# Optimization experiments

Measured on AMD Instinct MI355X. Metric: run time of the kernel, lower is better.

Reference implementation:

```python
import jax, jax.numpy as jnp
import numpy as np

D_MODEL = 1024
NUM_HEADS = 16
HEAD_DIM = D_MODEL // NUM_HEADS
FFN_HIDDEN = 4096
EPS = 1e-5


def setup_inputs() -> dict:
    key = jax.random.key(0)
    ks = jax.random.split(key, 7)
    s = 0.02
    return {
        "x": jax.random.normal(ks[0], (2, 2048, D_MODEL), dtype=jnp.float32),
        "W_qkv": jax.random.normal(ks[1], (D_MODEL, 3 * D_MODEL), dtype=jnp.float32) * s,
        "b_qkv": jnp.zeros((3 * D_MODEL,), dtype=jnp.float32),
        "W_o": jax.random.normal(ks[2], (D_MODEL, D_MODEL), dtype=jnp.float32) * s,
        "b_o": jnp.zeros((D_MODEL,), dtype=jnp.float32),
        "gamma1": jnp.ones((D_MODEL,), dtype=jnp.float32),
        "beta1": jnp.zeros((D_MODEL,), dtype=jnp.float32),
        "W1": jax.random.normal(ks[3], (D_MODEL, FFN_HIDDEN), dtype=jnp.float32) * s,
        "b1": jnp.zeros((FFN_HIDDEN,), dtype=jnp.float32),
        "W2": jax.random.normal(ks[4], (FFN_HIDDEN, D_MODEL), dtype=jnp.float32) * s,
        "b2": jnp.zeros((D_MODEL,), dtype=jnp.float32),
        "gamma2": jnp.ones((D_MODEL,), dtype=jnp.float32),
        "beta2": jnp.zeros((D_MODEL,), dtype=jnp.float32),
    }


def _layernorm(x, gamma, beta):
    mean = jnp.mean(x, axis=-1, keepdims=True)
    var = jnp.mean((x - mean) ** 2, axis=-1, keepdims=True)
    return gamma * (x - mean) / jnp.sqrt(var + EPS) + beta


def reference(x, W_qkv, b_qkv, W_o, b_o, gamma1, beta1, W1, b1, W2, b2, gamma2, beta2):
    B, S, D = x.shape
    # ---- multi-head attention ----
    qkv = x @ W_qkv + b_qkv                       # [B,S,3D]
    qkv = qkv.reshape(B, S, NUM_HEADS, 3 * HEAD_DIM).transpose(0, 2, 1, 3)  # [B,H,S,3hd]
    q, k, v = jnp.split(qkv, 3, axis=-1)          # each [B,H,S,hd]
    scores = jnp.einsum("bhqd,bhkd->bhqk", q, k) / np.sqrt(HEAD_DIM)
    attn = jax.nn.softmax(scores, axis=-1)
    vals = jnp.einsum("bhqk,bhkd->bhqd", attn, v)
    vals = vals.transpose(0, 2, 1, 3).reshape(B, S, D)
    attn_out = vals @ W_o + b_o
    # dropout disabled (eval mode)
    h = _layernorm(attn_out + x, gamma1, beta1)
    # ---- position-wise FFN (dropout before relu per source, disabled) ----
    ffn = jax.nn.relu(h @ W1 + b1) @ W2 + b2
    return _layernorm(ffn + h, gamma2, beta2)
```

## Files before the change

### kernel.cpp

```cpp
#include <hip/hip_runtime.h>
#include <stdint.h>

typedef float v4f __attribute__((ext_vector_type(4)));
typedef __bf16 v8bf __attribute__((ext_vector_type(8)));
typedef __bf16 v4bf __attribute__((ext_vector_type(4)));
typedef unsigned short v8us __attribute__((ext_vector_type(8)));
typedef unsigned short v4us __attribute__((ext_vector_type(4)));

__device__ __forceinline__ float b2f(unsigned short u) {
    union { float f; uint32_t i; } x; x.i = ((uint32_t)u) << 16; return x.f;
}
__device__ __forceinline__ unsigned short f2b(float f) {
    union { float f; uint32_t u; } x; x.f = f;
    uint32_t r = x.u + 0x7fffu + ((x.u >> 16) & 1u);
    return (unsigned short)(r >> 16);
}

__device__ __forceinline__ void gload16(const unsigned short* g, unsigned short* l) {
    __builtin_amdgcn_global_load_lds(
        (const __attribute__((address_space(1))) void*)g,
        (__attribute__((address_space(3))) void*)l,
        16, 0, 0);
}

__global__ __launch_bounds__(256) void convert_f32_bf16(
    const float* __restrict__ src, unsigned short* __restrict__ dst)
{
    int i = (blockIdx.x * 256 + threadIdx.x) * 4;
    float4 v = *(const float4*)&src[i];
    v4us o = {f2b(v.x), f2b(v.y), f2b(v.z), f2b(v.w)};
    *(v4us*)&dst[i] = o;
}

__global__ __launch_bounds__(256) void transpose_to_bt(
    const float* __restrict__ W, unsigned short* __restrict__ WT, int K, int N)
{
    __shared__ unsigned short t[64][65];
    const int kb = blockIdx.y * 64, nb = blockIdx.x * 64;
    const int r = threadIdx.x >> 4, c4 = (threadIdx.x & 15) * 4;
    #pragma unroll
    for (int i = 0; i < 4; ++i) {
        int k = r + i * 16;
        float4 v = *(const float4*)&W[(size_t)(kb + k) * N + nb + c4];
        t[c4 + 0][k] = f2b(v.x);
        t[c4 + 1][k] = f2b(v.y);
        t[c4 + 2][k] = f2b(v.z);
        t[c4 + 3][k] = f2b(v.w);
    }
    __syncthreads();
    #pragma unroll
    for (int i = 0; i < 4; ++i) {
        int n = r + i * 16;
        v4us o = {t[n][c4], t[n][c4 + 1], t[n][c4 + 2], t[n][c4 + 3]};
        *(v4us*)&WT[(size_t)(nb + n) * K + kb + c4] = o;
    }
}

__device__ __forceinline__ void xcd_swizzle(int& bm, int& bn) {
    int NB = gridDim.x, MB = gridDim.y;
    int flat = blockIdx.x + NB * blockIdx.y;
    int xcd = flat & 7, j = flat >> 3;
    int MBand = MB >> 3;
    bm = xcd * MBand + (j % MBand);
    bn = j / MBand;
}

template<int SPLIT_V>
__global__ __launch_bounds__(256) void gemm_bt(
    const unsigned short* __restrict__ A, const unsigned short* __restrict__ BT,
    const float* __restrict__ bias, unsigned short* __restrict__ C,
    unsigned short* __restrict__ VT, int M, int N, int K, int relu)
{
    __shared__ __align__(16) unsigned short sA[2][128 * 32];
    __shared__ __align__(16) unsigned short sB[2][128 * 32];
    const int tid  = threadIdx.x;
    const int wave = tid >> 6, lane = tid & 63;
    const int wm = wave >> 1, wn = wave & 1;
    const int quad = lane >> 4, l16 = lane & 15;
    int bm, bn;
    xcd_swizzle(bm, bn);

    const int srow = lane >> 2, scol = (lane & 3) * 8;
    const unsigned short* ga0 = A  + (size_t)(bm * 128 + (wave * 2 + 0) * 16 + srow) * K + scol;
    const unsigned short* ga1 = A  + (size_t)(bm * 128 + (wave * 2 + 1) * 16 + srow) * K + scol;
    const unsigned short* gb0 = BT + (size_t)(bn * 128 + (wave * 2 + 0) * 16 + srow) * K + scol;
    const unsigned short* gb1 = BT + (size_t)(bn * 128 + (wave * 2 + 1) * 16 + srow) * K + scol;
    const int o0 = (wave * 2 + 0) * 512 + lane * 8;
    const int o1 = (wave * 2 + 1) * 512 + lane * 8;

    v8us aR[2][2], bR[2][2];
    #pragma unroll
    for (int c = 0; c < 2; ++c) {
        aR[c][0] = *(const v8us*)(ga0 + c * 32);
        aR[c][1] = *(const v8us*)(ga1 + c * 32);
        bR[c][0] = *(const v8us*)(gb0 + c * 32);
        bR[c][1] = *(const v8us*)(gb1 + c * 32);
    }

    v4f acc[4][4];
    #pragma unroll
    for (int i = 0; i < 4; ++i)
        #pragma unroll
        for (int j = 0; j < 4; ++j)
            acc[i][j] = (v4f){0.f, 0.f, 0.f, 0.f};

    for (int kt = 0; kt < K; kt += 64) {
        __syncthreads();
        #pragma unroll
        for (int c = 0; c < 2; ++c) {
            *(v8us*)&sA[c][o0] = aR[c][0];
            *(v8us*)&sA[c][o1] = aR[c][1];
            *(v8us*)&sB[c][o0] = bR[c][0];
            *(v8us*)&sB[c][o1] = bR[c][1];
        }
        __syncthreads();
        if (kt + 64 < K) {
            int kn = kt + 64;
            #pragma unroll
            for (int c = 0; c < 2; ++c) {
                aR[c][0] = *(const v8us*)(ga0 + kn + c * 32);
                aR[c][1] = *(const v8us*)(ga1 + kn + c * 32);
                bR[c][0] = *(const v8us*)(gb0 + kn + c * 32);
                bR[c][1] = *(const v8us*)(gb1 + kn + c * 32);
            }
        }

        #pragma unroll
        for (int c = 0; c < 2; ++c) {
            v8bf af[4], bfr[4];
            #pragma unroll
            for (int mt = 0; mt < 4; ++mt)
                af[mt] = *(const v8bf*)&sA[c][(wm * 64 + mt * 16 + l16) * 32 + quad * 8];
            #pragma unroll
            for (int nt = 0; nt < 4; ++nt)
                bfr[nt] = *(const v8bf*)&sB[c][(wn * 64 + nt * 16 + l16) * 32 + quad * 8];
            #pragma unroll
            for (int mt = 0; mt < 4; ++mt)
                #pragma unroll
                for (int nt = 0; nt < 4; ++nt)
                    acc[mt][nt] = __builtin_amdgcn_mfma_f32_16x16x32_bf16(
                        af[mt], bfr[nt], acc[mt][nt], 0, 0, 0);
        }
    }

    #pragma unroll
    for (int mt = 0; mt < 4; ++mt) {
        int row = bm * 128 + wm * 64 + mt * 16 + quad * 4;
        #pragma unroll
        for (int nt = 0; nt < 4; ++nt) {
            int c0 = bn * 128 + wn * 64 + nt * 16;
            int col = c0 + l16;
            float bv = bias ? bias[col] : 0.f;
            if (SPLIT_V && (c0 % 192) >= 128) {
                int hh = c0 / 192;
                int d  = (c0 % 192) - 128 + l16;
                int bb = row >> 11;
                int s  = row & 2047;
                v4us st;
                #pragma unroll
                for (int r = 0; r < 4; ++r)
                    st[r] = f2b(acc[mt][nt][r] + bv);
                *(v4us*)&VT[((size_t)(bb * 16 + hh) * 64 + d) * 2048 + s] = st;
            } else {
                float qs = (SPLIT_V && (c0 % 192) < 64) ? 0.18033688f : 1.0f;
                #pragma unroll
                for (int r = 0; r < 4; ++r) {
                    float v = (acc[mt][nt][r] + bv) * qs;
                    if (relu) v = fmaxf(v, 0.f);
                    C[(size_t)(row + r) * N + col] = f2b(v);
                }
            }
        }
    }
}

__global__ __launch_bounds__(256) void gemm_bt_n64(
    const unsigned short* __restrict__ A, const unsigned short* __restrict__ BT,
    const float* __restrict__ bias, unsigned short* __restrict__ C,
    int M, int N, int K, int relu)
{
    __shared__ __align__(16) unsigned short sA[2][128 * 32];
    __shared__ __align__(16) unsigned short sB[2][64 * 32];
    const int tid  = threadIdx.x;
    const int wave = tid >> 6, lane = tid & 63;
    const int wm = wave >> 1, wn = wave & 1;
    const int quad = lane >> 4, l16 = lane & 15;
    int bm, bn;
    xcd_swizzle(bm, bn);

    const int srow = lane >> 2, scol = (lane & 3) * 8;
    const unsigned short* ga0 = A  + (size_t)(bm * 128 + (wave * 2 + 0) * 16 + srow) * K + scol;
    const unsigned short* ga1 = A  + (size_t)(bm * 128 + (wave * 2 + 1) * 16 + srow) * K + scol;
    const unsigned short* gb0 = BT + (size_t)(bn * 64 + wave * 16 + srow) * K + scol;
    const int oa0 = (wave * 2 + 0) * 512 + lane * 8;
    const int oa1 = (wave * 2 + 1) * 512 + lane * 8;
    const int ob  = wave * 512 + lane * 8;

    v8us aR[2][2], bR[2];
    #pragma unroll
    for (int c = 0; c < 2; ++c) {
        aR[c][0] = *(const v8us*)(ga0 + c * 32);
        aR[c][1] = *(const v8us*)(ga1 + c * 32);
        bR[c]    = *(const v8us*)(gb0 + c * 32);
    }

    v4f acc[4][2];
    #pragma unroll
    for (int i = 0; i < 4; ++i)
        #pragma unroll
        for (int j = 0; j < 2; ++j)
            acc[i][j] = (v4f){0.f, 0.f, 0.f, 0.f};

    for (int kt = 0; kt < K; kt += 64) {
        __syncthreads();
        #pragma unroll
        for (int c = 0; c < 2; ++c) {
            *(v8us*)&sA[c][oa0] = aR[c][0];
            *(v8us*)&sA[c][oa1] = aR[c][1];
            *(v8us*)&sB[c][ob]  = bR[c];
        }
        __syncthreads();
        if (kt + 64 < K) {
            int kn = kt + 64;
            #pragma unroll
            for (int c = 0; c < 2; ++c) {
                aR[c][0] = *(const v8us*)(ga0 + kn + c * 32);
                aR[c][1] = *(const v8us*)(ga1 + kn + c * 32);
                bR[c]    = *(const v8us*)(gb0 + kn + c * 32);
            }
        }

        #pragma unroll
        for (int c = 0; c < 2; ++c) {
            v8bf af[4], bfr[2];
            #pragma unroll
            for (int mt = 0; mt < 4; ++mt)
                af[mt] = *(const v8bf*)&sA[c][(wm * 64 + mt * 16 + l16) * 32 + quad * 8];
            #pragma unroll
            for (int nt = 0; nt < 2; ++nt)
                bfr[nt] = *(const v8bf*)&sB[c][(wn * 32 + nt * 16 + l16) * 32 + quad * 8];
            #pragma unroll
            for (int mt = 0; mt < 4; ++mt)
                #pragma unroll
                for (int nt = 0; nt < 2; ++nt)
                    acc[mt][nt] = __builtin_amdgcn_mfma_f32_16x16x32_bf16(
                        af[mt], bfr[nt], acc[mt][nt], 0, 0, 0);
        }
    }

    #pragma unroll
    for (int mt = 0; mt < 4; ++mt) {
        #pragma unroll
        for (int nt = 0; nt < 2; ++nt) {
            int col = bn * 64 + wn * 32 + nt * 16 + l16;
            float bv = bias ? bias[col] : 0.f;
            #pragma unroll
            for (int r = 0; r < 4; ++r) {
                int row = bm * 128 + wm * 64 + mt * 16 + quad * 4 + r;
                float v = acc[mt][nt][r] + bv;
                if (relu) v = fmaxf(v, 0.f);
                C[(size_t)row * N + col] = f2b(v);
            }
        }
    }
}

__global__ __launch_bounds__(512) void gemm256(
    const unsigned short* __restrict__ A, const unsigned short* __restrict__ BT,
    const float* __restrict__ bias, unsigned short* __restrict__ C,
    int M, int N, int K, int relu)
{
    __shared__ __align__(16) unsigned short sA[2][256 * 64];
    __shared__ __align__(16) unsigned short sB[2][256 * 64];
    const int tid  = threadIdx.x;
    const int wave = tid >> 6, lane = tid & 63;
    const int wm = wave >> 2, wn = wave & 3;
    const int quad = lane >> 4, l16 = lane & 15;
    int bm, bn;
    xcd_swizzle(bm, bn);

    const int srow = lane >> 3;
    const int scol = ((lane & 7) * 8) ^ ((lane & 32) ? 16 : 0);
    size_t aoff[4], boff[4];
    #pragma unroll
    for (int j = 0; j < 4; ++j) {
        int r = wave * 32 + j * 8 + srow;
        aoff[j] = (size_t)(bm * 256 + r) * K + scol;
        boff[j] = (size_t)(bn * 256 + r) * K + scol;
    }
    const int lds0 = wave * 32 * 64;

    const int ksw = (quad * 8) ^ ((l16 & 4) ? 16 : 0);

    v4f acc[8][4];
    #pragma unroll
    for (int i = 0; i < 8; ++i)
        #pragma unroll
        for (int j = 0; j < 4; ++j)
            acc[i][j] = (v4f){0.f, 0.f, 0.f, 0.f};

    const int NT = K >> 6;
    #pragma unroll
    for (int j = 0; j < 4; ++j) {
        gload16(A  + aoff[j], &sA[0][lds0 + j * 512]);
        gload16(BT + boff[j], &sB[0][lds0 + j * 512]);
    }
    __syncthreads();

    for (int t = 0; t < NT; ++t) {
        const int buf = t & 1;
        if (t + 1 < NT) {
            const int ktn = (t + 1) << 6;
            #pragma unroll
            for (int j = 0; j < 4; ++j) {
                gload16(A  + aoff[j] + ktn, &sA[buf ^ 1][lds0 + j * 512]);
                gload16(BT + boff[j] + ktn, &sB[buf ^ 1][lds0 + j * 512]);
            }
        }

        v8bf bfr[4][2];
        #pragma unroll
        for (int nt2 = 0; nt2 < 4; ++nt2)
            #pragma unroll
            for (int kc = 0; kc < 2; ++kc)
                bfr[nt2][kc] = *(const v8bf*)&sB[buf][
                    (wn * 64 + nt2 * 16 + l16) * 64 + kc * 32 + ksw];
        #pragma unroll
        for (int mq = 0; mq < 2; ++mq) {
            v8bf af[4][2];
            #pragma unroll
            for (int mt2 = 0; mt2 < 4; ++mt2)
                #pragma unroll
                for (int kc = 0; kc < 2; ++kc)
                    af[mt2][kc] = *(const v8bf*)&sA[buf][
                        (wm * 128 + mq * 64 + mt2 * 16 + l16) * 64 + kc * 32 + ksw];
            #pragma unroll
            for (int mt2 = 0; mt2 < 4; ++mt2)
                #pragma unroll
                for (int nt2 = 0; nt2 < 4; ++nt2)
                    #pragma unroll
                    for (int kc = 0; kc < 2; ++kc)
                        acc[mq * 4 + mt2][nt2] =
                            __builtin_amdgcn_mfma_f32_16x16x32_bf16(
                                af[mt2][kc], bfr[nt2][kc],
                                acc[mq * 4 + mt2][nt2], 0, 0, 0);
        }
        __syncthreads();
    }

    #pragma unroll
    for (int mt = 0; mt < 8; ++mt) {
        int row = bm * 256 + wm * 128 + mt * 16 + quad * 4;
        #pragma unroll
        for (int nt = 0; nt < 4; ++nt) {
            int col = bn * 256 + wn * 64 + nt * 16 + l16;
            float bv = bias ? bias[col] : 0.f;
            #pragma unroll
            for (int r = 0; r < 4; ++r) {
                float v = acc[mt][nt][r] + bv;
                if (relu) v = fmaxf(v, 0.f);
                C[(size_t)(row + r) * N + col] = f2b(v);
            }
        }
    }
}

__global__ __launch_bounds__(256) void attn_mfma(
    const unsigned short* __restrict__ qkv, const unsigned short* __restrict__ VT,
    unsigned short* __restrict__ av)
{
    __shared__ __align__(16) unsigned short sK[64 * 72];
    __shared__ __align__(16) unsigned short sVT[64 * 72];
    __shared__ __align__(16) unsigned short sP[4][32 * 72];
    const int tid  = threadIdx.x;
    const int wave = tid >> 6, lane = tid & 63;
    const int quad = lane >> 4, l16 = lane & 15;
    const int blk = blockIdx.x;
    const int xcd = blk & 7, local = blk >> 3;
    const int bh = xcd * 4 + (local & 3);
    const int qb = local >> 2;
    const int h = bh & 15, b = bh >> 4;
    const int row0 = b * 2048;
    const int qbase = row0 + qb * 128 + wave * 32;
    const size_t qoff = (size_t)h * 192;
    const size_t koff = qoff + 64;

    v8bf qf[2][2];
    #pragma unroll
    for (int qt = 0; qt < 2; ++qt)
        #pragma unroll
        for (int kc = 0; kc < 2; ++kc)
            qf[qt][kc] = *(const v8bf*)&qkv[(size_t)(qbase + qt * 16 + l16) * 3072
                                            + qoff + kc * 32 + quad * 8];

    v4f o[4][2];
    #pragma unroll
    for (int dt = 0; dt < 4; ++dt)
        #pragma unroll
        for (int qt = 0; qt < 2; ++qt)
            o[dt][qt] = (v4f){0.f, 0.f, 0.f, 0.f};
    float ll[2] = {0.f, 0.f};

    const int k_key0 = tid >> 3,        k_oct = (tid & 7) * 8;
    const int k_key1 = (tid + 256) >> 3;
    const int v_d0 = tid >> 3,          v_koct = (tid & 7) * 8;
    const int v_d1 = (tid + 256) >> 3;
    const unsigned short* gK0 = qkv + (size_t)(row0 + k_key0) * 3072 + koff + k_oct;
    const unsigned short* gK1 = qkv + (size_t)(row0 + k_key1) * 3072 + koff + k_oct;
    const unsigned short* gV0 = VT + ((size_t)bh * 64 + v_d0) * 2048 + v_koct;
    const unsigned short* gV1 = VT + ((size_t)bh * 64 + v_d1) * 2048 + v_koct;
    const size_t stepK = (size_t)64 * 3072;
    const size_t stepV = 64;

    v8us kreg0 = *(const v8us*)gK0, kreg1 = *(const v8us*)gK1;
    v8us vreg0 = *(const v8us*)gV0, vreg1 = *(const v8us*)gV1;
    gK0 += stepK; gK1 += stepK; gV0 += stepV; gV1 += stepV;

    for (int kt = 0; kt < 32; ++kt) {
        __syncthreads();
        *(v8us*)&sK[k_key0 * 72 + k_oct] = kreg0;
        *(v8us*)&sK[k_key1 * 72 + k_oct] = kreg1;
        *(v8us*)&sVT[v_d0 * 72 + v_koct] = vreg0;
        *(v8us*)&sVT[v_d1 * 72 + v_koct] = vreg1;
        __syncthreads();
        if (kt < 31) {
            kreg0 = *(const v8us*)gK0; kreg1 = *(const v8us*)gK1;
            vreg0 = *(const v8us*)gV0; vreg1 = *(const v8us*)gV1;
            gK0 += stepK; gK1 += stepK; gV0 += stepV; gV1 += stepV;
        }

        v4f sc[4][2];
        #pragma unroll
        for (int kk = 0; kk < 4; ++kk) {
            #pragma unroll
            for (int qt = 0; qt < 2; ++qt)
                sc[kk][qt] = (v4f){0.f, 0.f, 0.f, 0.f};
            #pragma unroll
            for (int kc = 0; kc < 2; ++kc) {
                v8bf ak = *(const v8bf*)&sK[(kk * 16 + l16) * 72 + kc * 32 + quad * 8];
                #pragma unroll
                for (int qt = 0; qt < 2; ++qt)
                    sc[kk][qt] = __builtin_amdgcn_mfma_f32_16x16x32_bf16(
                        ak, qf[qt][kc], sc[kk][qt], 0, 0, 0);
            }
        }

        #pragma unroll
        for (int qt = 0; qt < 2; ++qt) {
            float ps = 0.f;
            #pragma unroll
            for (int kk = 0; kk < 4; ++kk) {
                v4bf pk;
                #pragma unroll
                for (int rr = 0; rr < 4; ++rr) {
                    float p = __builtin_amdgcn_exp2f(sc[kk][qt][rr]);
                    ps += p;
                    pk[rr] = (__bf16)p;
                }
                *(v4bf*)&sP[wave][(qt * 16 + l16) * 72 + kk * 16 + quad * 4] = pk;
            }
            ll[qt] += ps;
        }

        __asm__ volatile("s_waitcnt lgkmcnt(0)" ::: "memory");

        #pragma unroll
        for (int c = 0; c < 2; ++c) {
            v8bf pb[2];
            #pragma unroll
            for (int qt = 0; qt < 2; ++qt) {
                union { v8bf v; v8us u; } u;
                u.u = *(const v8us*)&sP[wave][(qt * 16 + l16) * 72 + c * 32 + quad * 8];
                pb[qt] = u.v;
            }
            #pragma unroll
            for (int dt = 0; dt < 4; ++dt) {
                v8bf va = *(const v8bf*)&sVT[(dt * 16 + l16) * 72 + c * 32 + quad * 8];
                #pragma unroll
                for (int qt = 0; qt < 2; ++qt)
                    o[dt][qt] = __builtin_amdgcn_mfma_f32_16x16x32_bf16(
                        va, pb[qt], o[dt][qt], 0, 0, 0);
            }
        }
    }

    #pragma unroll
    for (int qt = 0; qt < 2; ++qt) {
        float l = ll[qt];
        l += __shfl_xor(l, 16, 64);
        l += __shfl_xor(l, 32, 64);
        float inv = 1.f / l;
        int qrow = qbase + qt * 16 + l16;
        #pragma unroll
        for (int dt = 0; dt < 4; ++dt) {
            v4bf st;
            #pragma unroll
            for (int rr = 0; rr < 4; ++rr)
                st[rr] = (__bf16)(o[dt][qt][rr] * inv);
            *(v4bf*)&av[(size_t)qrow * 1024 + h * 64 + dt * 16 + quad * 4] = st;
        }
    }
}

template<int RES_F32, int OUT_F32>
__global__ __launch_bounds__(256) void ln_fused(
    const unsigned short* __restrict__ a, const void* __restrict__ residv,
    const float* __restrict__ gamma, const float* __restrict__ beta,
    void* __restrict__ outv)
{
    const int row = blockIdx.x, tid = threadIdx.x;
    const size_t base = (size_t)row * 1024;
    const int c0 = tid * 4;
    ushort4 avv = *(const ushort4*)&a[base + c0];
    float y[4];
    if (RES_F32) {
        float4 rv = *(const float4*)((const float*)residv + base + c0);
        y[0] = b2f(avv.x) + rv.x;
        y[1] = b2f(avv.y) + rv.y;
        y[2] = b2f(avv.z) + rv.z;
        y[3] = b2f(avv.w) + rv.w;
    } else {
        ushort4 rv = *(const ushort4*)((const unsigned short*)residv + base + c0);
        y[0] = b2f(avv.x) + b2f(rv.x);
        y[1] = b2f(avv.y) + b2f(rv.y);
        y[2] = b2f(avv.z) + b2f(rv.z);
        y[3] = b2f(avv.w) + b2f(rv.w);
    }
    float s  = y[0] + y[1] + y[2] + y[3];
    float ss = y[0]*y[0] + y[1]*y[1] + y[2]*y[2] + y[3]*y[3];
    #pragma unroll
    for (int off = 32; off; off >>= 1) {
        s  += __shfl_xor(s, off, 64);
        ss += __shfl_xor(ss, off, 64);
    }
    __shared__ float red[8];
    int wave = tid >> 6, lane = tid & 63;
    if (lane == 0) { red[wave] = s; red[4 + wave] = ss; }
    __syncthreads();
    s  = red[0] + red[1] + red[2] + red[3];
    ss = red[4] + red[5] + red[6] + red[7];
    float mean = s * (1.f / 1024.f);
    float var  = ss * (1.f / 1024.f) - mean * mean;
    float rstd = rsqrtf(var + 1e-5f);
    float4 gv = *(const float4*)&gamma[c0];
    float4 bv = *(const float4*)&beta[c0];
    float r0 = gv.x * (y[0] - mean) * rstd + bv.x;
    float r1 = gv.y * (y[1] - mean) * rstd + bv.y;
    float r2 = gv.z * (y[2] - mean) * rstd + bv.z;
    float r3 = gv.w * (y[3] - mean) * rstd + bv.w;
    if (OUT_F32) {
        float4 ov = {r0, r1, r2, r3};
        *(float4*)((float*)outv + base + c0) = ov;
    } else {
        ushort4 ov;
        ov.x = f2b(r0); ov.y = f2b(r1); ov.z = f2b(r2); ov.w = f2b(r3);
        *(ushort4*)((unsigned short*)outv + base + c0) = ov;
    }
}

extern "C" void kernel_launch(void* const* d_in, const int* in_sizes, int n_in,
                              void* d_out, int out_size, void* d_ws, size_t ws_size,
                              hipStream_t stream)
{
    (void)in_sizes; (void)n_in; (void)out_size; (void)ws_size;
    const float* x    = (const float*)d_in[0];
    const float* Wqkv = (const float*)d_in[1];
    const float* bqkv = (const float*)d_in[2];
    const float* Wo   = (const float*)d_in[3];
    const float* bo   = (const float*)d_in[4];
    const float* g1   = (const float*)d_in[5];
    const float* be1  = (const float*)d_in[6];
    const float* W1   = (const float*)d_in[7];
    const float* b1   = (const float*)d_in[8];
    const float* W2   = (const float*)d_in[9];
    const float* b2   = (const float*)d_in[10];
    const float* g2   = (const float*)d_in[11];
    const float* be2  = (const float*)d_in[12];
    float* out = (float*)d_out;

    unsigned short* R0 = (unsigned short*)d_ws;
    unsigned short* R1 = R0 + (size_t)16 * 1024 * 1024;
    unsigned short* R2 = R1 + (size_t)4 * 1024 * 1024;
    unsigned short* R3 = R2 + (size_t)4 * 1024 * 1024;
    unsigned short* WqkvT = R0 + (size_t)12 * 1024 * 1024;

    const int M = 4096;
    dim3 blk(256);

    convert_f32_bf16<<<dim3(M * 1024 / 1024), blk, 0, stream>>>(x, R2);
    transpose_to_bt<<<dim3(48, 16), blk, 0, stream>>>(Wqkv, WqkvT, 1024, 3072);
    gemm_bt<1><<<dim3(24, 32), blk, 0, stream>>>(R2, WqkvT, bqkv, R0, R1, M, 3072, 1024, 0);
    attn_mfma<<<dim3(512), blk, 0, stream>>>(R0, R1, R3);
    transpose_to_bt<<<dim3(16, 16), blk, 0, stream>>>(Wo, R2, 1024, 1024);
    gemm_bt_n64<<<dim3(16, 32), blk, 0, stream>>>(R3, R2, bo, R1, M, 1024, 1024, 0);
    ln_fused<1, 0><<<dim3(4096), blk, 0, stream>>>(R1, x, g1, be1, R2);
    transpose_to_bt<<<dim3(64, 16), blk, 0, stream>>>(W1, R3, 1024, 4096);
    gemm256<<<dim3(16, 16), dim3(512), 0, stream>>>(R2, R3, b1, R0, M, 4096, 1024, 1);
    transpose_to_bt<<<dim3(16, 64), blk, 0, stream>>>(W2, R1, 4096, 1024);
    gemm_bt_n64<<<dim3(16, 32), blk, 0, stream>>>(R0, R1, b2, R3, M, 1024, 4096, 0);
    ln_fused<0, 1><<<dim3(4096), blk, 0, stream>>>(R3, R2, g2, be2, out);
}
```

Measured before the change: 347.0 us.

## Split attention query tile across eight waves of sixteen rows each

The attention kernel now launches 512 threads per block, with each of eight waves handling 16 query rows instead of four waves handling 32. Each thread loads one K and one V chunk per tile instead of two. This halves per-wave accumulator and register use and doubles the waves available to hide MFMA and LDS latency. In exchange, each K/V fragment read from shared memory feeds only one MFMA instead of two, so LDS read traffic per unit of compute roughly doubles.

```diff
diff --git a/kernel.cpp b/kernel.cpp
--- a/kernel.cpp
+++ b/kernel.cpp
@@ -365,13 +365,13 @@
     }
 }
 
-__global__ __launch_bounds__(256) void attn_mfma(
+__global__ __launch_bounds__(512) void attn_mfma(
     const unsigned short* __restrict__ qkv, const unsigned short* __restrict__ VT,
     unsigned short* __restrict__ av)
 {
     __shared__ __align__(16) unsigned short sK[64 * 72];
     __shared__ __align__(16) unsigned short sVT[64 * 72];
-    __shared__ __align__(16) unsigned short sP[4][32 * 72];
+    __shared__ __align__(16) unsigned short sP[8][16 * 72];
     const int tid  = threadIdx.x;
     const int wave = tid >> 6, lane = tid & 63;
     const int quad = lane >> 4, l16 = lane & 15;
@@ -381,124 +381,97 @@
     const int qb = local >> 2;
     const int h = bh & 15, b = bh >> 4;
     const int row0 = b * 2048;
-    const int qbase = row0 + qb * 128 + wave * 32;
+    const int qbase = row0 + qb * 128 + wave * 16;
     const size_t qoff = (size_t)h * 192;
     const size_t koff = qoff + 64;
 
-    v8bf qf[2][2];
-    #pragma unroll
-    for (int qt = 0; qt < 2; ++qt)
-        #pragma unroll
-        for (int kc = 0; kc < 2; ++kc)
-            qf[qt][kc] = *(const v8bf*)&qkv[(size_t)(qbase + qt * 16 + l16) * 3072
-                                            + qoff + kc * 32 + quad * 8];
-
-    v4f o[4][2];
+    v8bf qf[2];
+    #pragma unroll
+    for (int kc = 0; kc < 2; ++kc)
+        qf[kc] = *(const v8bf*)&qkv[(size_t)(qbase + l16) * 3072
+                                    + qoff + kc * 32 + quad * 8];
+
+    v4f o[4];
     #pragma unroll
     for (int dt = 0; dt < 4; ++dt)
-        #pragma unroll
-        for (int qt = 0; qt < 2; ++qt)
-            o[dt][qt] = (v4f){0.f, 0.f, 0.f, 0.f};
-    float ll[2] = {0.f, 0.f};
-
-    const int k_key0 = tid >> 3,        k_oct = (tid & 7) * 8;
-    const int k_key1 = (tid + 256) >> 3;
-    const int v_d0 = tid >> 3,          v_koct = (tid & 7) * 8;
-    const int v_d1 = (tid + 256) >> 3;
-    const unsigned short* gK0 = qkv + (size_t)(row0 + k_key0) * 3072 + koff + k_oct;
-    const unsigned short* gK1 = qkv + (size_t)(row0 + k_key1) * 3072 + koff + k_oct;
-    const unsigned short* gV0 = VT + ((size_t)bh * 64 + v_d0) * 2048 + v_koct;
-    const unsigned short* gV1 = VT + ((size_t)bh * 64 + v_d1) * 2048 + v_koct;
+        o[dt] = (v4f){0.f, 0.f, 0.f, 0.f};
+    float ll = 0.f;
+
+    const int k_key = tid >> 3, k_oct = (tid & 7) * 8;
+    const unsigned short* gK = qkv + (size_t)(row0 + k_key) * 3072 + koff + k_oct;
+    const unsigned short* gV = VT + ((size_t)bh * 64 + k_key) * 2048 + k_oct;
     const size_t stepK = (size_t)64 * 3072;
     const size_t stepV = 64;
 
-    v8us kreg0 = *(const v8us*)gK0, kreg1 = *(const v8us*)gK1;
-    v8us vreg0 = *(const v8us*)gV0, vreg1 = *(const v8us*)gV1;
-    gK0 += stepK; gK1 += stepK; gV0 += stepV; gV1 += stepV;
+    v8us kreg = *(const v8us*)gK;
+    v8us vreg = *(const v8us*)gV;
+    gK += stepK; gV += stepV;
 
     for (int kt = 0; kt < 32; ++kt) {
         __syncthreads();
-        *(v8us*)&sK[k_key0 * 72 + k_oct] = kreg0;
-        *(v8us*)&sK[k_key1 * 72 + k_oct] = kreg1;
-        *(v8us*)&sVT[v_d0 * 72 + v_koct] = vreg0;
-        *(v8us*)&sVT[v_d1 * 72 + v_koct] = vreg1;
+        *(v8us*)&sK[k_key * 72 + k_oct]  = kreg;
+        *(v8us*)&sVT[k_key * 72 + k_oct] = vreg;
         __syncthreads();
         if (kt < 31) {
-            kreg0 = *(const v8us*)gK0; kreg1 = *(const v8us*)gK1;
-            vreg0 = *(const v8us*)gV0; vreg1 = *(const v8us*)gV1;
-            gK0 += stepK; gK1 += stepK; gV0 += stepV; gV1 += stepV;
-        }
-
-        v4f sc[4][2];
+            kreg = *(const v8us*)gK;
+            vreg = *(const v8us*)gV;
+            gK += stepK; gV += stepV;
+        }
+
+        v4f sc[4];
         #pragma unroll
         for (int kk = 0; kk < 4; ++kk) {
-            #pragma unroll
-            for (int qt = 0; qt < 2; ++qt)
-                sc[kk][qt] = (v4f){0.f, 0.f, 0.f, 0.f};
+            sc[kk] = (v4f){0.f, 0.f, 0.f, 0.f};
             #pragma unroll
             for (int kc = 0; kc < 2; ++kc) {
                 v8bf ak = *(const v8bf*)&sK[(kk * 16 + l16) * 72 + kc * 32 + quad * 8];
-                #pragma unroll
-                for (int qt = 0; qt < 2; ++qt)
-                    sc[kk][qt] = __builtin_amdgcn_mfma_f32_16x16x32_bf16(
-                        ak, qf[qt][kc], sc[kk][qt], 0, 0, 0);
-            }
-        }
-
-        #pragma unroll
-        for (int qt = 0; qt < 2; ++qt) {
-            float ps = 0.f;
-            #pragma unroll
-            for (int kk = 0; kk < 4; ++kk) {
-                v4bf pk;
-                #pragma unroll
-                for (int rr = 0; rr < 4; ++rr) {
-                    float p = __builtin_amdgcn_exp2f(sc[kk][qt][rr]);
-                    ps += p;
-                    pk[rr] = (__bf16)p;
-                }
-                *(v4bf*)&sP[wave][(qt * 16 + l16) * 72 + kk * 16 + quad * 4] = pk;
-            }
-            ll[qt] += ps;
-        }
+                sc[kk] = __builtin_amdgcn_mfma_f32_16x16x32_bf16(
+                    ak, qf[kc], sc[kk], 0, 0, 0);
+            }
+        }
+
+        float ps = 0.f;
+        #pragma unroll
+        for (int kk = 0; kk < 4; ++kk) {
+            v4bf pk;
+            #pragma unroll
+            for (int rr = 0; rr < 4; ++rr) {
+                float p = __builtin_amdgcn_exp2f(sc[kk][rr]);
+                ps += p;
+                pk[rr] = (__bf16)p;
+            }
+            *(v4bf*)&sP[wave][l16 * 72 + kk * 16 + quad * 4] = pk;
+        }
+        ll += ps;
 
         __asm__ volatile("s_waitcnt lgkmcnt(0)" ::: "memory");
 
         #pragma unroll
         for (int c = 0; c < 2; ++c) {
-            v8bf pb[2];
-            #pragma unroll
-            for (int qt = 0; qt < 2; ++qt) {
-                union { v8bf v; v8us u; } u;
-                u.u = *(const v8us*)&sP[wave][(qt * 16 + l16) * 72 + c * 32 + quad * 8];
-                pb[qt] = u.v;
-            }
+            union { v8bf v; v8us u; } u;
+            u.u = *(const v8us*)&sP[wave][l16 * 72 + c * 32 + quad * 8];
+            v8bf pb = u.v;
             #pragma unroll
             for (int dt = 0; dt < 4; ++dt) {
                 v8bf va = *(const v8bf*)&sVT[(dt * 16 + l16) * 72 + c * 32 + quad * 8];
-                #pragma unroll
-                for (int qt = 0; qt < 2; ++qt)
-                    o[dt][qt] = __builtin_amdgcn_mfma_f32_16x16x32_bf16(
-                        va, pb[qt], o[dt][qt], 0, 0, 0);
-            }
-        }
-    }
-
-    #pragma unroll
-    for (int qt = 0; qt < 2; ++qt) {
-        float l = ll[qt];
-        l += __shfl_xor(l, 16, 64);
-        l += __shfl_xor(l, 32, 64);
-        float inv = 1.f / l;
-        int qrow = qbase + qt * 16 + l16;
-        #pragma unroll
-        for (int dt = 0; dt < 4; ++dt) {
-            v4bf st;
-            #pragma unroll
-            for (int rr = 0; rr < 4; ++rr)
-                st[rr] = (__bf16)(o[dt][qt][rr] * inv);
-            *(v4bf*)&av[(size_t)qrow * 1024 + h * 64 + dt * 16 + quad * 4] = st;
-        }
+                o[dt] = __builtin_amdgcn_mfma_f32_16x16x32_bf16(
+                    va, pb, o[dt], 0, 0, 0);
+            }
+        }
+    }
+
+    float l = ll;
+    l += __shfl_xor(l, 16, 64);
+    l += __shfl_xor(l, 32, 64);
+    float inv = 1.f / l;
+    int qrow = qbase + l16;
+    #pragma unroll
+    for (int dt = 0; dt < 4; ++dt) {
+        v4bf st;
+        #pragma unroll
+        for (int rr = 0; rr < 4; ++rr)
+            st[rr] = (__bf16)(o[dt][rr] * inv);
+        *(v4bf*)&av[(size_t)qrow * 1024 + h * 64 + dt * 16 + quad * 4] = st;
     }
 }
 
@@ -590,7 +563,7 @@
     convert_f32_bf16<<<dim3(M * 1024 / 1024), blk, 0, stream>>>(x, R2);
     transpose_to_bt<<<dim3(48, 16), blk, 0, stream>>>(Wqkv, WqkvT, 1024, 3072);
     gemm_bt<1><<<dim3(24, 32), blk, 0, stream>>>(R2, WqkvT, bqkv, R0, R1, M, 3072, 1024, 0);
-    attn_mfma<<<dim3(512), blk, 0, stream>>>(R0, R1, R3);
+    attn_mfma<<<dim3(512), dim3(512), 0, stream>>>(R0, R1, R3);
     transpose_to_bt<<<dim3(16, 16), blk, 0, stream>>>(Wo, R2, 1024, 1024);
     gemm_bt_n64<<<dim3(16, 32), blk, 0, stream>>>(R3, R2, bo, R1, M, 1024, 1024, 0);
     ln_fused<1, 0><<<dim3(4096), blk, 0, stream>>>(R1, x, g1, be1, R2);
```

Result: no change. 350.0 us (+0.9%).
